# Optimization experiments

Measured on AMD Instinct MI355X. Metric: run time of the kernel, lower is better.

The kernel has to match this reference:

```python
import jax, jax.numpy as jnp
import numpy as np

MEM_DIM = 2048
BATCH = 4096


def setup_inputs() -> dict:
    key = jax.random.key(0)
    ks = jax.random.split(key, 8)
    D = MEM_DIM
    scale = 1.0 / np.sqrt(D)  # torch nn.Linear default init range ~ U(-1/sqrt(D), 1/sqrt(D))
    lc = jax.random.normal(ks[0], (BATCH, D), dtype=jnp.float32)
    lh = jax.random.normal(ks[1], (BATCH, D), dtype=jnp.float32)
    rc = jax.random.normal(ks[2], (BATCH, D), dtype=jnp.float32)
    rh = jax.random.normal(ks[3], (BATCH, D), dtype=jnp.float32)
    # Fused params: columns [0:D]=input gate, [D:2D]=left forget, [2D:3D]=right forget, [3D:4D]=update
    Wl = jax.random.uniform(ks[4], (D, 4 * D), dtype=jnp.float32, minval=-scale, maxval=scale)
    Wr = jax.random.uniform(ks[5], (D, 4 * D), dtype=jnp.float32, minval=-scale, maxval=scale)
    bl = jax.random.uniform(ks[6], (4 * D,), dtype=jnp.float32, minval=-scale, maxval=scale)
    br = jax.random.uniform(ks[7], (4 * D,), dtype=jnp.float32, minval=-scale, maxval=scale)
    return {"lc": lc, "lh": lh, "rc": rc, "rh": rh, "Wl": Wl, "bl": bl, "Wr": Wr, "br": br}


def reference(lc, lh, rc, rh, Wl, bl, Wr, br):
    D = lh.shape[-1]
    # Two fused GEMMs replace 8 separate mem_dim x mem_dim linears (same math).
    g = jnp.dot(lh, Wl) + bl + jnp.dot(rh, Wr) + br  # [B, 4D]
    i = jax.nn.sigmoid(g[:, 0 * D:1 * D])   # input gate
    lf = jax.nn.sigmoid(g[:, 1 * D:2 * D])  # left forget gate
    rf = jax.nn.sigmoid(g[:, 2 * D:3 * D])  # right forget gate
    u = jnp.tanh(g[:, 3 * D:4 * D])         # cell update
    c = i * u + lf * lc + rf * rc
    h = jnp.tanh(c)
    return (c, h)
```

## Files before the change

### kernel.cpp

```cpp
#include <hip/hip_runtime.h>
#include <stdint.h>

#define D_MEM 2048
#define BATCH 4096
#define K_DIM 4096
#define N_DIM 8192

typedef __bf16 bf16x8 __attribute__((ext_vector_type(8)));
typedef float f32x4 __attribute__((ext_vector_type(4)));

typedef const void __attribute__((address_space(1)))* gas_t;
typedef void __attribute__((address_space(3)))* las_t;

__device__ __forceinline__ ushort f2b(float f) {
  union { float f; uint32_t u; } v; v.f = f;
  uint32_t u = v.u + 0x7fffu + ((v.u >> 16) & 1u);
  return (ushort)(u >> 16);
}
__device__ __forceinline__ float b2f(ushort s) {
  union { uint32_t u; float f; } v; v.u = ((uint32_t)s) << 16;
  return v.f;
}
__device__ __forceinline__ float sigm(float x) {
  return 1.0f / (1.0f + __expf(-x));
}
__device__ __forceinline__ float tanh_fast(float x) {
  return __builtin_fmaf(2.0f, sigm(2.0f * x), -1.0f);
}

__global__ void cast_concat_kernel(const float* __restrict__ lh,
                                   const float* __restrict__ rh,
                                   ushort* __restrict__ A) {
  int i4 = blockIdx.x * 256 + threadIdx.x;
  int row = i4 >> 10;
  int col = (i4 & 1023) * 4;
  const float* src = (col < D_MEM) ? (lh + (size_t)row * D_MEM + col)
                                   : (rh + (size_t)row * D_MEM + (col - D_MEM));
  float4 v = *(const float4*)src;
  ushort4 o; o.x = f2b(v.x); o.y = f2b(v.y); o.z = f2b(v.z); o.w = f2b(v.w);
  *(ushort4*)(A + (size_t)row * K_DIM + col) = o;
}

__global__ void transpose_cast_kernel(const float* __restrict__ Wl,
                                      const float* __restrict__ Wr,
                                      ushort* __restrict__ Bt) {
  __shared__ float t[64 * 65];
  const float* W = blockIdx.z ? Wr : Wl;
  int n0 = blockIdx.x * 64;
  int k0 = blockIdx.y * 64;
  int tid = threadIdx.x;
#pragma unroll
  for (int i = 0; i < 4; ++i) {
    int idx = i * 256 + tid;
    int rr = idx >> 4;
    int c4 = (idx & 15) * 4;
    float4 v = *(const float4*)(W + (size_t)(k0 + rr) * N_DIM + n0 + c4);
    t[rr * 65 + c4 + 0] = v.x;
    t[rr * 65 + c4 + 1] = v.y;
    t[rr * 65 + c4 + 2] = v.z;
    t[rr * 65 + c4 + 3] = v.w;
  }
  __syncthreads();
  int kbase = (blockIdx.z ? D_MEM : 0) + k0;
#pragma unroll
  for (int i = 0; i < 4; ++i) {
    int idx = i * 256 + tid;
    int rr = idx >> 4;
    int c4 = (idx & 15) * 4;
    ushort4 o;
    o.x = f2b(t[(c4 + 0) * 65 + rr]);
    o.y = f2b(t[(c4 + 1) * 65 + rr]);
    o.z = f2b(t[(c4 + 2) * 65 + rr]);
    o.w = f2b(t[(c4 + 3) * 65 + rr]);
    *(ushort4*)(Bt + (size_t)(n0 + rr) * K_DIM + kbase + c4) = o;
  }
}

__device__ __forceinline__ void stage2(const ushort* g0, const ushort* g1,
                                       char* dst, int wave) {
  __builtin_amdgcn_global_load_lds((gas_t)g0, (las_t)(dst + wave * 1024), 16, 0, 0);
  __builtin_amdgcn_global_load_lds((gas_t)g1, (las_t)(dst + 8192 + wave * 1024), 16, 0, 0);
}

#define PHASE(MH, KS, BUF, G0, G1, LDST, DOVM)                                 \
  do {                                                                         \
    bf16x8 af[4];                                                              \
    {                                                                          \
      const char* ab_ = AsB + (BUF)*32768 + (KS)*16384;                        \
      _Pragma("unroll") for (int f_ = 0; f_ < 4; ++f_)                         \
          af[f_] = *(const bf16x8*)(ab_ + aoff[MH][f_]);                       \
      if ((MH) == 0) {                                                         \
        const char* bb_ = BsB + (BUF)*32768 + (KS)*16384;                      \
        _Pragma("unroll") for (int j_ = 0; j_ < 4; ++j_)                       \
            bfr[j_] = *(const bf16x8*)(bb_ + boff[j_]);                        \
      }                                                                        \
    }                                                                          \
    stage2((G0), (G1), (LDST), wave);                                          \
    __builtin_amdgcn_s_barrier();                                              \
    asm volatile("s_waitcnt lgkmcnt(0)" ::: "memory");                         \
    __builtin_amdgcn_sched_barrier(0);                                         \
    __builtin_amdgcn_s_setprio(1);                                             \
    _Pragma("unroll") for (int i_ = 0; i_ < 4; ++i_)                           \
        _Pragma("unroll") for (int j_ = 0; j_ < 4; ++j_)                       \
            acc[(MH)*4 + i_][j_] = __builtin_amdgcn_mfma_f32_16x16x32_bf16(    \
                af[i_], bfr[j_], acc[(MH)*4 + i_][j_], 0, 0, 0);               \
    __builtin_amdgcn_s_setprio(0);                                             \
    if (DOVM) asm volatile("s_waitcnt vmcnt(8)" ::: "memory");                 \
    __builtin_amdgcn_s_barrier();                                              \
  } while (0)

__global__ __launch_bounds__(512, 2) void gemm_bf16_kernel(
    const ushort* __restrict__ A,
    const ushort* __restrict__ B,
    ushort* __restrict__ C) {
  __shared__ char smem[131072];
  char* AsB = smem;
  char* BsB = smem + 65536;
  const int K = K_DIM, N = N_DIM;

  int tid = threadIdx.x;
  int lane = tid & 63, wave = tid >> 6;
  int wm = wave >> 2, wn = wave & 3;
  int q = lane >> 4, r = lane & 15;

  int bid = blockIdx.x;
  int swz = (bid & 7) * 64 + (bid >> 3);
  int m0 = (swz >> 5) * 256;
  int n0 = (swz & 31) * 256;

  int ci0 = tid, ci1 = 512 + tid;
  int r0 = ci0 >> 2, c0 = (ci0 & 3) ^ ((r0 ^ (r0 >> 2)) & 3);
  int r1 = ci1 >> 2, c1 = (ci1 & 3) ^ ((r1 ^ (r1 >> 2)) & 3);
  const ushort* sA0 = A + (size_t)(m0 + r0) * K + c0 * 8;
  const ushort* sA1 = A + (size_t)(m0 + r1) * K + c1 * 8;
  const ushort* sB0 = B + (size_t)(n0 + r0) * K + c0 * 8;
  const ushort* sB1 = B + (size_t)(n0 + r1) * K + c1 * 8;

  int swzr = (r ^ (r >> 2)) & 3;
  int aoff[2][4], boff[4];
#pragma unroll
  for (int mh = 0; mh < 2; ++mh)
#pragma unroll
    for (int f = 0; f < 4; ++f) {
      int row = wm * 128 + mh * 64 + f * 16 + r;
      aoff[mh][f] = row * 64 + (q ^ swzr) * 16;
    }
#pragma unroll
  for (int j = 0; j < 4; ++j) {
    int col = wn * 64 + j * 16 + r;
    boff[j] = col * 64 + (q ^ swzr) * 16;
  }

  f32x4 acc[8][4];
#pragma unroll
  for (int i = 0; i < 8; ++i)
#pragma unroll
    for (int j = 0; j < 4; ++j) acc[i][j] = f32x4{0.f, 0.f, 0.f, 0.f};
  bf16x8 bfr[4];

  stage2(sA0,      sA1,      AsB + 0,     wave);
  stage2(sB0,      sB1,      BsB + 0,     wave);
  stage2(sA0 + 32, sA1 + 32, AsB + 16384, wave);
  stage2(sB0 + 32, sB1 + 32, BsB + 16384, wave);
  stage2(sA0 + 64, sA1 + 64, AsB + 32768, wave);
  stage2(sB0 + 64, sB1 + 64, BsB + 32768, wave);
  asm volatile("s_waitcnt vmcnt(8)" ::: "memory");
  __builtin_amdgcn_s_barrier();

#pragma unroll 1
  for (int t = 0; t < 64; t += 2) {
    const int o1 = (t + 1) * 64;
    const int o2 = (t + 2 < 64 ? t + 2 : 63) * 64;
    const int o3 = (t + 3 < 64 ? t + 3 : 63) * 64;
    PHASE(0, 0, 0, sA0 + o1 + 32, sA1 + o1 + 32, AsB + 49152, 0);
    PHASE(1, 0, 0, sB0 + o1 + 32, sB1 + o1 + 32, BsB + 49152, 1);
    PHASE(0, 1, 0, sA0 + o2,      sA1 + o2,      AsB + 0,     0);
    PHASE(1, 1, 0, sB0 + o2,      sB1 + o2,      BsB + 0,     1);
    PHASE(0, 0, 1, sA0 + o2 + 32, sA1 + o2 + 32, AsB + 16384, 0);
    PHASE(1, 0, 1, sB0 + o2 + 32, sB1 + o2 + 32, BsB + 16384, 1);
    PHASE(0, 1, 1, sA0 + o3,      sA1 + o3,      AsB + 32768, 0);
    PHASE(1, 1, 1, sB0 + o3,      sB1 + o3,      BsB + 32768, 1);
  }

#pragma unroll
  for (int i = 0; i < 8; ++i) {
    int gm_base = m0 + wm * 128 + i * 16 + q * 4;
#pragma unroll
    for (int j = 0; j < 4; ++j) {
      int gn = n0 + wn * 64 + j * 16 + r;
      size_t base = (size_t)gm_base * N + gn;
#pragma unroll
      for (int e = 0; e < 4; ++e)
        C[base + (size_t)e * N] = f2b(acc[i][j][e]);
    }
  }
}

__global__ void gate_kernel(const ushort* __restrict__ G,
                            const float* __restrict__ bl,
                            const float* __restrict__ br,
                            const float* __restrict__ lc,
                            const float* __restrict__ rc,
                            float* __restrict__ out) {
  int i4 = blockIdx.x * 256 + threadIdx.x;
  int row = i4 >> 9;
  int col = (i4 & 511) * 4;
  size_t gbase = (size_t)row * N_DIM + col;

  ushort4 ui = *(const ushort4*)(G + gbase);
  ushort4 uf = *(const ushort4*)(G + gbase + 1 * D_MEM);
  ushort4 ug = *(const ushort4*)(G + gbase + 2 * D_MEM);
  ushort4 uu = *(const ushort4*)(G + gbase + 3 * D_MEM);

  float4 bli = *(const float4*)(bl + col);
  float4 blf = *(const float4*)(bl + col + 1 * D_MEM);
  float4 blr = *(const float4*)(bl + col + 2 * D_MEM);
  float4 blu = *(const float4*)(bl + col + 3 * D_MEM);
  float4 bri = *(const float4*)(br + col);
  float4 brf = *(const float4*)(br + col + 1 * D_MEM);
  float4 brr = *(const float4*)(br + col + 2 * D_MEM);
  float4 bru = *(const float4*)(br + col + 3 * D_MEM);

  float4 vlc = *(const float4*)(lc + (size_t)row * D_MEM + col);
  float4 vrc = *(const float4*)(rc + (size_t)row * D_MEM + col);

  float4 vc, vh;
  {
    float gi = b2f(ui.x) + bli.x + bri.x;
    float gf = b2f(uf.x) + blf.x + brf.x;
    float gr = b2f(ug.x) + blr.x + brr.x;
    float gu = b2f(uu.x) + blu.x + bru.x;
    vc.x = sigm(gi) * tanh_fast(gu) + sigm(gf) * vlc.x + sigm(gr) * vrc.x;
    vh.x = tanh_fast(vc.x);
  }
  {
    float gi = b2f(ui.y) + bli.y + bri.y;
    float gf = b2f(uf.y) + blf.y + brf.y;
    float gr = b2f(ug.y) + blr.y + brr.y;
    float gu = b2f(uu.y) + blu.y + bru.y;
    vc.y = sigm(gi) * tanh_fast(gu) + sigm(gf) * vlc.y + sigm(gr) * vrc.y;
    vh.y = tanh_fast(vc.y);
  }
  {
    float gi = b2f(ui.z) + bli.z + bri.z;
    float gf = b2f(uf.z) + blf.z + brf.z;
    float gr = b2f(ug.z) + blr.z + brr.z;
    float gu = b2f(uu.z) + blu.z + bru.z;
    vc.z = sigm(gi) * tanh_fast(gu) + sigm(gf) * vlc.z + sigm(gr) * vrc.z;
    vh.z = tanh_fast(vc.z);
  }
  {
    float gi = b2f(ui.w) + bli.w + bri.w;
    float gf = b2f(uf.w) + blf.w + brf.w;
    float gr = b2f(ug.w) + blr.w + brr.w;
    float gu = b2f(uu.w) + blu.w + bru.w;
    vc.w = sigm(gi) * tanh_fast(gu) + sigm(gf) * vlc.w + sigm(gr) * vrc.w;
    vh.w = tanh_fast(vc.w);
  }

  size_t obase = (size_t)row * D_MEM + col;
  *(float4*)(out + obase) = vc;
  *(float4*)(out + (size_t)BATCH * D_MEM + obase) = vh;
}

extern "C" void kernel_launch(void* const* d_in, const int* in_sizes, int n_in,
                              void* d_out, int out_size, void* d_ws, size_t ws_size,
                              hipStream_t stream) {
  const float* lc = (const float*)d_in[0];
  const float* lh = (const float*)d_in[1];
  const float* rc = (const float*)d_in[2];
  const float* rh = (const float*)d_in[3];
  const float* Wl = (const float*)d_in[4];
  const float* bl = (const float*)d_in[5];
  const float* Wr = (const float*)d_in[6];
  const float* br = (const float*)d_in[7];
  float* out = (float*)d_out;

  char* ws = (char*)d_ws;
  ushort* A  = (ushort*)ws;
  ushort* Bt = (ushort*)(ws + (size_t)32 * 1024 * 1024);
  ushort* G  = (ushort*)(ws + (size_t)96 * 1024 * 1024);

  cast_concat_kernel<<<16384, 256, 0, stream>>>(lh, rh, A);
  dim3 tg(128, 32, 2);
  transpose_cast_kernel<<<tg, 256, 0, stream>>>(Wl, Wr, Bt);
  gemm_bf16_kernel<<<512, 512, 0, stream>>>(A, Bt, G);
  gate_kernel<<<8192, 256, 0, stream>>>(G, bl, br, lc, rc, out);
}
```

Measured before the change: 546.6 us.

## Merge GEMM phase pairs into half-steps with a single barrier each

Each pair of per-M-half phases becomes one step. The step issues both A and B async global-to-LDS loads, reads all A and B fragments, runs 32 MFMAs, then waits on vmcnt and hits a single barrier. This halves the barrier count and drops the mid-phase barrier and lgkmcnt wait, so the scheduler can interleave LDS reads with MFMAs. The cost is more live fragment registers and reliance on compiler-inserted LDS waits, which may hurt occupancy or leave less slack for the async stage to overlap.

```diff
diff --git a/kernel.cpp b/kernel.cpp
--- a/kernel.cpp
+++ b/kernel.cpp
@@ -82,30 +82,30 @@
   __builtin_amdgcn_global_load_lds((gas_t)g1, (las_t)(dst + 8192 + wave * 1024), 16, 0, 0);
 }
 
-#define PHASE(MH, KS, BUF, G0, G1, LDST, DOVM)                                 \
+#define HALF(KS, BUF, GA0, GA1, DSTA, GB0, GB1, DSTB)                          \
   do {                                                                         \
-    bf16x8 af[4];                                                              \
-    {                                                                          \
-      const char* ab_ = AsB + (BUF)*32768 + (KS)*16384;                        \
-      _Pragma("unroll") for (int f_ = 0; f_ < 4; ++f_)                         \
-          af[f_] = *(const bf16x8*)(ab_ + aoff[MH][f_]);                       \
-      if ((MH) == 0) {                                                         \
-        const char* bb_ = BsB + (BUF)*32768 + (KS)*16384;                      \
-        _Pragma("unroll") for (int j_ = 0; j_ < 4; ++j_)                       \
-            bfr[j_] = *(const bf16x8*)(bb_ + boff[j_]);                        \
-      }                                                                        \
-    }                                                                          \
-    stage2((G0), (G1), (LDST), wave);                                          \
-    __builtin_amdgcn_s_barrier();                                              \
-    asm volatile("s_waitcnt lgkmcnt(0)" ::: "memory");                         \
-    __builtin_amdgcn_sched_barrier(0);                                         \
+    stage2((GA0), (GA1), (DSTA), wave);                                        \
+    stage2((GB0), (GB1), (DSTB), wave);                                        \
+    bf16x8 af0[4], af1[4], bq[4];                                              \
+    const char* ab_ = AsB + (BUF)*32768 + (KS)*16384;                          \
+    const char* bb_ = BsB + (BUF)*32768 + (KS)*16384;                          \
+    _Pragma("unroll") for (int f_ = 0; f_ < 4; ++f_)                           \
+        af0[f_] = *(const bf16x8*)(ab_ + aoff[0][f_]);                         \
+    _Pragma("unroll") for (int j_ = 0; j_ < 4; ++j_)                           \
+        bq[j_] = *(const bf16x8*)(bb_ + boff[j_]);                             \
+    _Pragma("unroll") for (int f_ = 0; f_ < 4; ++f_)                           \
+        af1[f_] = *(const bf16x8*)(ab_ + aoff[1][f_]);                         \
     __builtin_amdgcn_s_setprio(1);                                             \
     _Pragma("unroll") for (int i_ = 0; i_ < 4; ++i_)                           \
         _Pragma("unroll") for (int j_ = 0; j_ < 4; ++j_)                       \
-            acc[(MH)*4 + i_][j_] = __builtin_amdgcn_mfma_f32_16x16x32_bf16(    \
-                af[i_], bfr[j_], acc[(MH)*4 + i_][j_], 0, 0, 0);               \
+            acc[i_][j_] = __builtin_amdgcn_mfma_f32_16x16x32_bf16(             \
+                af0[i_], bq[j_], acc[i_][j_], 0, 0, 0);                        \
+    _Pragma("unroll") for (int i_ = 0; i_ < 4; ++i_)                           \
+        _Pragma("unroll") for (int j_ = 0; j_ < 4; ++j_)                       \
+            acc[4 + i_][j_] = __builtin_amdgcn_mfma_f32_16x16x32_bf16(         \
+                af1[i_], bq[j_], acc[4 + i_][j_], 0, 0, 0);                    \
     __builtin_amdgcn_s_setprio(0);                                             \
-    if (DOVM) asm volatile("s_waitcnt vmcnt(8)" ::: "memory");                 \
+    asm volatile("s_waitcnt vmcnt(8)" ::: "memory");                           \
     __builtin_amdgcn_s_barrier();                                              \
   } while (0)
 
@@ -156,7 +156,6 @@
   for (int i = 0; i < 8; ++i)
 #pragma unroll
     for (int j = 0; j < 4; ++j) acc[i][j] = f32x4{0.f, 0.f, 0.f, 0.f};
-  bf16x8 bfr[4];
 
   stage2(sA0,      sA1,      AsB + 0,     wave);
   stage2(sB0,      sB1,      BsB + 0,     wave);
@@ -172,14 +171,14 @@
     const int o1 = (t + 1) * 64;
     const int o2 = (t + 2 < 64 ? t + 2 : 63) * 64;
     const int o3 = (t + 3 < 64 ? t + 3 : 63) * 64;
-    PHASE(0, 0, 0, sA0 + o1 + 32, sA1 + o1 + 32, AsB + 49152, 0);
-    PHASE(1, 0, 0, sB0 + o1 + 32, sB1 + o1 + 32, BsB + 49152, 1);
-    PHASE(0, 1, 0, sA0 + o2,      sA1 + o2,      AsB + 0,     0);
-    PHASE(1, 1, 0, sB0 + o2,      sB1 + o2,      BsB + 0,     1);
-    PHASE(0, 0, 1, sA0 + o2 + 32, sA1 + o2 + 32, AsB + 16384, 0);
-    PHASE(1, 0, 1, sB0 + o2 + 32, sB1 + o2 + 32, BsB + 16384, 1);
-    PHASE(0, 1, 1, sA0 + o3,      sA1 + o3,      AsB + 32768, 0);
-    PHASE(1, 1, 1, sB0 + o3,      sB1 + o3,      BsB + 32768, 1);
+    HALF(0, 0, sA0 + o1 + 32, sA1 + o1 + 32, AsB + 49152,
+               sB0 + o1 + 32, sB1 + o1 + 32, BsB + 49152);
+    HALF(1, 0, sA0 + o2,      sA1 + o2,      AsB + 0,
+               sB0 + o2,      sB1 + o2,      BsB + 0);
+    HALF(0, 1, sA0 + o2 + 32, sA1 + o2 + 32, AsB + 16384,
+               sB0 + o2 + 32, sB1 + o2 + 32, BsB + 16384);
+    HALF(1, 1, sA0 + o3,      sA1 + o3,      AsB + 32768,
+               sB0 + o3,      sB1 + o3,      BsB + 32768);
   }
 
 #pragma unroll
```

Measured after the change: 540.8 us. Within noise of the previous version (-1.1%).
